# Performance work log

Measured on AMD Instinct MI355X. Metric: run time of the kernel, lower is better.

Reference implementation:

```python
import jax, jax.numpy as jnp
import numpy as np

B, T, D, HD = 256, 256, 512, 64  # batch, seq_len(SEQ_LEN), EMBED_DIM, head_dim


def setup_inputs() -> dict:
    key = jax.random.key(0)
    k1, k2, k3, k4 = jax.random.split(key, 4)
    scale = D ** -0.5  # roughly matches nn.Linear init variance
    return {
        "x": jax.random.normal(k1, (B, T, D), dtype=jnp.float32),
        "Wq": jax.random.normal(k2, (HD, D), dtype=jnp.float32) * scale,
        "Wk": jax.random.normal(k3, (HD, D), dtype=jnp.float32) * scale,
        "Wv": jax.random.normal(k4, (HD, D), dtype=jnp.float32) * scale,
    }


def reference(x, Wq, Wk, Wv):
    # q,k,v: [B, T, HD]  (torch Linear: x @ W.T, no bias)
    q = jnp.einsum("btd,hd->bth", x, Wq)
    k = jnp.einsum("btd,hd->bth", x, Wk)
    v = jnp.einsum("btd,hd->bth", x, Wv)
    head_dim = Wq.shape[0]
    # scores: [B, T, T], scaled by head_dim^-0.5
    scores = jnp.einsum("bqh,bkh->bqk", q, k) * (head_dim ** -0.5)
    T_ = x.shape[1]
    causal = jnp.tril(jnp.ones((T_, T_), dtype=bool))  # tril[:T,:T] == 0 -> -inf
    scores = jnp.where(causal, scores, -jnp.inf)
    attn = jax.nn.softmax(scores, axis=-1)
    # dropout is identity in eval mode (reference baseline)
    return jnp.einsum("bqk,bkh->bqh", attn, v)
```

## Files before the change

kernel.cpp:

```cpp
#include <hip/hip_runtime.h>
#include <hip/hip_bf16.h>
#include <stdint.h>

#define NB 256
#define NT 256
#define ND 512
#define NH 64

typedef __bf16 bf16;
typedef __bf16 bf16x4 __attribute__((ext_vector_type(4)));
typedef __bf16 bf16x8 __attribute__((ext_vector_type(8)));
typedef float f32x4 __attribute__((ext_vector_type(4)));

static __device__ __forceinline__ f32x4 mfma16(bf16x8 a, bf16x8 b, f32x4 c) {
    return __builtin_amdgcn_mfma_f32_16x16x32_bf16(a, b, c, 0, 0, 0);
}

static __device__ __forceinline__ bf16x8 cvt8(f32x4 a, f32x4 b) {
    bf16x8 r;
    r[0] = (bf16)a.x; r[1] = (bf16)a.y; r[2] = (bf16)a.z; r[3] = (bf16)a.w;
    r[4] = (bf16)b.x; r[5] = (bf16)b.y; r[6] = (bf16)b.z; r[7] = (bf16)b.w;
    return r;
}

__global__ __launch_bounds__(256) void wconv_kernel(
        const float* __restrict__ Wq, const float* __restrict__ Wk,
        const float* __restrict__ Wv, bf16* __restrict__ wbf) {
    int idx = (blockIdx.x * 256 + threadIdx.x) * 4;
    const float* src;
    if (idx < 64 * ND)       src = Wq + idx;
    else if (idx < 128 * ND) src = Wk + (idx - 64 * ND);
    else                     src = Wv + (idx - 128 * ND);
    f32x4 v = *reinterpret_cast<const f32x4*>(src);
    bf16x4 o;
    o[0] = (bf16)v.x; o[1] = (bf16)v.y; o[2] = (bf16)v.z; o[3] = (bf16)v.w;
    *reinterpret_cast<bf16x4*>(wbf + idx) = o;
}

__global__ __launch_bounds__(256) void qkv_gemm_kernel(
        const float* __restrict__ x, const bf16* __restrict__ wbf,
        bf16* __restrict__ qws, bf16* __restrict__ kws, bf16* __restrict__ vt) {
    __shared__ alignas(16) char lds[16384];
    const int t = threadIdx.x;
    const int lane = t & 63, wave = t >> 6;
    const long m0 = (long)blockIdx.x * 64;

    const int srow = t >> 2, skc = (t & 3) * 16;
    const int ssw = (srow & 7) << 4;
    const int sbase = srow * 128 + skc * 2;
    const float* xsrc = x + (m0 + srow) * ND + skc;

    f32x4 acc[4][3] = {};

    {
        f32x4 a = *reinterpret_cast<const f32x4*>(xsrc);
        f32x4 b = *reinterpret_cast<const f32x4*>(xsrc + 4);
        f32x4 c = *reinterpret_cast<const f32x4*>(xsrc + 8);
        f32x4 d = *reinterpret_cast<const f32x4*>(xsrc + 12);
        *reinterpret_cast<bf16x8*>(lds + (sbase ^ ssw)) = cvt8(a, b);
        *reinterpret_cast<bf16x8*>(lds + ((sbase + 16) ^ ssw)) = cvt8(c, d);
    }
    __syncthreads();

    #pragma unroll
    for (int kk = 0; kk < ND; kk += 64) {
        char* cbuf = lds + ((kk >> 6) & 1) * 8192;
        char* nbuf = lds + ((((kk >> 6) & 1)) ^ 1) * 8192;
        f32x4 xa, xb, xc, xd;
        const bool have_next = (kk + 64) < ND;
        if (have_next) {
            const float* s2 = xsrc + kk + 64;
            xa = *reinterpret_cast<const f32x4*>(s2);
            xb = *reinterpret_cast<const f32x4*>(s2 + 4);
            xc = *reinterpret_cast<const f32x4*>(s2 + 8);
            xd = *reinterpret_cast<const f32x4*>(s2 + 12);
        }
        #pragma unroll
        for (int k2 = 0; k2 < 2; ++k2) {
            const int koff = (k2 * 32 + (lane >> 4) * 8) * 2;
            const int kg = kk + k2 * 32 + (lane >> 4) * 8;
            bf16x8 Af[4];
            #pragma unroll
            for (int ri = 0; ri < 4; ++ri) {
                int row = ri * 16 + (lane & 15);
                Af[ri] = *reinterpret_cast<const bf16x8*>(
                    cbuf + ((row * 128 + koff) ^ ((row & 7) << 4)));
            }
            #pragma unroll
            for (int ci = 0; ci < 3; ++ci) {
                int n = wave * 48 + ci * 16 + (lane & 15);
                bf16x8 Bf = *reinterpret_cast<const bf16x8*>(wbf + n * ND + kg);
                #pragma unroll
                for (int ri = 0; ri < 4; ++ri)
                    acc[ri][ci] = mfma16(Af[ri], Bf, acc[ri][ci]);
            }
        }
        if (have_next) {
            *reinterpret_cast<bf16x8*>(nbuf + (sbase ^ ssw)) = cvt8(xa, xb);
            *reinterpret_cast<bf16x8*>(nbuf + ((sbase + 16) ^ ssw)) = cvt8(xc, xd);
        }
        __syncthreads();
    }

    const int b = blockIdx.x >> 2;
    const int tb = (blockIdx.x & 3) * 64;
    #pragma unroll
    for (int ci = 0; ci < 3; ++ci) {
        int n = wave * 48 + ci * 16 + (lane & 15);
        int sel = n >> 6, hd = n & 63;
        #pragma unroll
        for (int ri = 0; ri < 4; ++ri) {
            #pragma unroll
            for (int r = 0; r < 4; ++r) {
                int trow = tb + ri * 16 + (lane >> 4) * 4 + r;
                long grow = m0 + ri * 16 + (lane >> 4) * 4 + r;
                float val = acc[ri][ci][r];
                if (sel == 0)      qws[grow * NH + hd] = (bf16)(val * 0.125f);
                else if (sel == 1) kws[grow * NH + hd] = (bf16)val;
                else               vt[((long)b * NH + hd) * NT + trow] = (bf16)val;
            }
        }
    }
}

__global__ __launch_bounds__(256) void attn_kernel(
        const bf16* __restrict__ qws, const bf16* __restrict__ kws,
        const bf16* __restrict__ vt, float* __restrict__ out) {
    __shared__ alignas(16) char lds[32768];
    const int t = threadIdx.x, lane = t & 63, wave = t >> 6;
    const int qb = blockIdx.x, b = blockIdx.y;
    const long bbase = (long)b * NT;

    const int ncolt = qb * 4 + wave + 1;
    const int ncolt2 = (ncolt + 1) & ~1;

    bf16x8 Qf[2];
    {
        long qrow = bbase + qb * 64 + wave * 16 + (lane & 15);
        const bf16* qsrc = qws + qrow * NH + (lane >> 4) * 8;
        Qf[0] = *reinterpret_cast<const bf16x8*>(qsrc);
        Qf[1] = *reinterpret_cast<const bf16x8*>(qsrc + 32);
    }

    f32x4 S[16] = {};
    #pragma unroll
    for (int c = 0; c < 16; ++c) {
        if (c < ncolt2) {
            const bf16* kbase = kws + (bbase + c * 16 + (lane & 15)) * NH + (lane >> 4) * 8;
            S[c] = mfma16(Qf[0], *reinterpret_cast<const bf16x8*>(kbase), S[c]);
            S[c] = mfma16(Qf[1], *reinterpret_cast<const bf16x8*>(kbase + 32), S[c]);
        }
    }

    const int qrow0 = qb * 64 + wave * 16 + (lane >> 4) * 4;
    float sum[4] = {0.f, 0.f, 0.f, 0.f};
    #pragma unroll
    for (int c = 0; c < 16; ++c) {
        if (c < ncolt2) {
            int col = c * 16 + (lane & 15);
            #pragma unroll
            for (int r = 0; r < 4; ++r) {
                float p = (col <= qrow0 + r) ? __expf(S[c][r]) : 0.0f;
                S[c][r] = p;
                sum[r] += p;
            }
        }
    }
    #pragma unroll
    for (int r = 0; r < 4; ++r) {
        sum[r] += __shfl_xor(sum[r], 1);
        sum[r] += __shfl_xor(sum[r], 2);
        sum[r] += __shfl_xor(sum[r], 4);
        sum[r] += __shfl_xor(sum[r], 8);
    }

    char* plds = lds + wave * 8192;
    #pragma unroll
    for (int c = 0; c < 16; ++c) {
        if (c < ncolt2) {
            int colp = c * 16 + (lane & 15);
            #pragma unroll
            for (int r = 0; r < 4; ++r) {
                int rowp = (lane >> 4) * 4 + r;
                *reinterpret_cast<bf16*>(plds + ((rowp * 512 + colp * 2) ^ ((rowp & 7) << 4))) =
                    (bf16)S[c][r];
            }
        }
    }

    f32x4 O[4] = {};
    #pragma unroll
    for (int kk2 = 0; kk2 < 8; ++kk2) {
        if (kk2 < (ncolt2 >> 1)) {
            const int kv0 = kk2 * 32 + (lane >> 4) * 8;
            const int rowp = lane & 15;
            bf16x8 Pf = *reinterpret_cast<const bf16x8*>(
                plds + ((rowp * 512 + kv0 * 2) ^ ((rowp & 7) << 4)));
            #pragma unroll
            for (int cb = 0; cb < 4; ++cb) {
                int hd = cb * 16 + (lane & 15);
                bf16x8 Vf = *reinterpret_cast<const bf16x8*>(
                    vt + ((long)b * NH + hd) * NT + kv0);
                O[cb] = mfma16(Pf, Vf, O[cb]);
            }
        }
    }

    float rinv[4];
    #pragma unroll
    for (int r = 0; r < 4; ++r) rinv[r] = 1.0f / sum[r];

    #pragma unroll
    for (int cb = 0; cb < 4; ++cb) {
        int hd = cb * 16 + (lane & 15);
        #pragma unroll
        for (int r = 0; r < 4; ++r) {
            long orow = bbase + qb * 64 + wave * 16 + (lane >> 4) * 4 + r;
            out[orow * NH + hd] = O[cb][r] * rinv[r];
        }
    }
}

extern "C" void kernel_launch(void* const* d_in, const int* in_sizes, int n_in,
                              void* d_out, int out_size, void* d_ws, size_t ws_size,
                              hipStream_t stream) {
    const float* x  = (const float*)d_in[0];
    const float* Wq = (const float*)d_in[1];
    const float* Wk = (const float*)d_in[2];
    const float* Wv = (const float*)d_in[3];
    float* out = (float*)d_out;

    char* ws = (char*)d_ws;
    bf16* wbf = (bf16*)ws;
    bf16* qws = (bf16*)(ws + 0x30000);
    bf16* kws = (bf16*)(ws + 0x30000 + 8388608);
    bf16* vt  = (bf16*)(ws + 0x30000 + 2 * 8388608);

    wconv_kernel<<<96, 256, 0, stream>>>(Wq, Wk, Wv, wbf);
    qkv_gemm_kernel<<<1024, 256, 0, stream>>>(x, wbf, qws, kws, vt);
    attn_kernel<<<dim3(4, NB), 256, 0, stream>>>(qws, kws, vt, out);
}
```

Measured before the change: 261.9 us.

## Stage full x tile in LDS for QKV GEMM; split attention into one-wave blocks

The QKV projection now loads and converts the whole 64x512 x tile into a 64KB LDS buffer up front, then runs the MFMA loop with no per-step barriers, replacing the double-buffered loop. The attention kernel now launches one 64-thread block per 16-row query tile (16x256 grid) and fuses scoring, exp, P staging and PV accumulation into one chunked loop, avoiding the 16-register score array. This is meant to cut synchronisation and register pressure and to balance the causal workload across more blocks. The 64KB LDS allocation limits GEMM occupancy, and the staging loses overlap of the load with compute.

```diff
diff --git a/kernel.cpp b/kernel.cpp
--- a/kernel.cpp
+++ b/kernel.cpp
@@ -40,73 +40,56 @@
 __global__ __launch_bounds__(256) void qkv_gemm_kernel(
         const float* __restrict__ x, const bf16* __restrict__ wbf,
         bf16* __restrict__ qws, bf16* __restrict__ kws, bf16* __restrict__ vt) {
-    __shared__ alignas(16) char lds[16384];
+    __shared__ alignas(16) char lds[65536];
     const int t = threadIdx.x;
     const int lane = t & 63, wave = t >> 6;
     const long m0 = (long)blockIdx.x * 64;
 
-    const int srow = t >> 2, skc = (t & 3) * 16;
-    const int ssw = (srow & 7) << 4;
-    const int sbase = srow * 128 + skc * 2;
-    const float* xsrc = x + (m0 + srow) * ND + skc;
+    {
+        const int srow = t >> 2, skc = (t & 3) * 16;
+        const int ssw = (srow & 7) << 4;
+        const float* xsrc = x + (m0 + srow) * ND + skc;
+        #pragma unroll
+        for (int kk = 0; kk < ND; kk += 64) {
+            f32x4 a = *reinterpret_cast<const f32x4*>(xsrc + kk);
+            f32x4 b = *reinterpret_cast<const f32x4*>(xsrc + kk + 4);
+            f32x4 c = *reinterpret_cast<const f32x4*>(xsrc + kk + 8);
+            f32x4 d = *reinterpret_cast<const f32x4*>(xsrc + kk + 12);
+            int base = srow * 1024 + (kk + skc) * 2;
+            *reinterpret_cast<bf16x8*>(lds + (base ^ ssw)) = cvt8(a, b);
+            *reinterpret_cast<bf16x8*>(lds + ((base + 16) ^ ssw)) = cvt8(c, d);
+        }
+    }
+    __syncthreads();
 
     f32x4 acc[4][3] = {};
-
-    {
-        f32x4 a = *reinterpret_cast<const f32x4*>(xsrc);
-        f32x4 b = *reinterpret_cast<const f32x4*>(xsrc + 4);
-        f32x4 c = *reinterpret_cast<const f32x4*>(xsrc + 8);
-        f32x4 d = *reinterpret_cast<const f32x4*>(xsrc + 12);
-        *reinterpret_cast<bf16x8*>(lds + (sbase ^ ssw)) = cvt8(a, b);
-        *reinterpret_cast<bf16x8*>(lds + ((sbase + 16) ^ ssw)) = cvt8(c, d);
-    }
-    __syncthreads();
-
-    #pragma unroll
-    for (int kk = 0; kk < ND; kk += 64) {
-        char* cbuf = lds + ((kk >> 6) & 1) * 8192;
-        char* nbuf = lds + ((((kk >> 6) & 1)) ^ 1) * 8192;
-        f32x4 xa, xb, xc, xd;
-        const bool have_next = (kk + 64) < ND;
-        if (have_next) {
-            const float* s2 = xsrc + kk + 64;
-            xa = *reinterpret_cast<const f32x4*>(s2);
-            xb = *reinterpret_cast<const f32x4*>(s2 + 4);
-            xc = *reinterpret_cast<const f32x4*>(s2 + 8);
-            xd = *reinterpret_cast<const f32x4*>(s2 + 12);
-        }
-        #pragma unroll
-        for (int k2 = 0; k2 < 2; ++k2) {
-            const int koff = (k2 * 32 + (lane >> 4) * 8) * 2;
-            const int kg = kk + k2 * 32 + (lane >> 4) * 8;
-            bf16x8 Af[4];
-            #pragma unroll
-            for (int ri = 0; ri < 4; ++ri) {
-                int row = ri * 16 + (lane & 15);
-                Af[ri] = *reinterpret_cast<const bf16x8*>(
-                    cbuf + ((row * 128 + koff) ^ ((row & 7) << 4)));
-            }
-            #pragma unroll
-            for (int ci = 0; ci < 3; ++ci) {
-                int n = wave * 48 + ci * 16 + (lane & 15);
-                bf16x8 Bf = *reinterpret_cast<const bf16x8*>(wbf + n * ND + kg);
-                #pragma unroll
-                for (int ri = 0; ri < 4; ++ri)
-                    acc[ri][ci] = mfma16(Af[ri], Bf, acc[ri][ci]);
-            }
-        }
-        if (have_next) {
-            *reinterpret_cast<bf16x8*>(nbuf + (sbase ^ ssw)) = cvt8(xa, xb);
-            *reinterpret_cast<bf16x8*>(nbuf + ((sbase + 16) ^ ssw)) = cvt8(xc, xd);
-        }
-        __syncthreads();
+    const int l15 = lane & 15, g8 = (lane >> 4) * 8;
+
+    #pragma unroll 4
+    for (int chunk = 0; chunk < 16; ++chunk) {
+        const int kg = chunk * 32 + g8;
+        bf16x8 Af[4];
+        #pragma unroll
+        for (int ri = 0; ri < 4; ++ri) {
+            int row = ri * 16 + l15;
+            Af[ri] = *reinterpret_cast<const bf16x8*>(
+                lds + ((row * 1024 + kg * 2) ^ ((row & 7) << 4)));
+        }
+        #pragma unroll
+        for (int ci = 0; ci < 3; ++ci) {
+            int n = wave * 48 + ci * 16 + l15;
+            bf16x8 Bf = *reinterpret_cast<const bf16x8*>(wbf + n * ND + kg);
+            #pragma unroll
+            for (int ri = 0; ri < 4; ++ri)
+                acc[ri][ci] = mfma16(Af[ri], Bf, acc[ri][ci]);
+        }
     }
 
     const int b = blockIdx.x >> 2;
     const int tb = (blockIdx.x & 3) * 64;
     #pragma unroll
     for (int ci = 0; ci < 3; ++ci) {
-        int n = wave * 48 + ci * 16 + (lane & 15);
+        int n = wave * 48 + ci * 16 + l15;
         int sel = n >> 6, hd = n & 63;
         #pragma unroll
         for (int ri = 0; ri < 4; ++ri) {
@@ -123,100 +106,87 @@
     }
 }
 
-__global__ __launch_bounds__(256) void attn_kernel(
+__global__ __launch_bounds__(64) void attn_kernel(
         const bf16* __restrict__ qws, const bf16* __restrict__ kws,
         const bf16* __restrict__ vt, float* __restrict__ out) {
-    __shared__ alignas(16) char lds[32768];
-    const int t = threadIdx.x, lane = t & 63, wave = t >> 6;
-    const int qb = blockIdx.x, b = blockIdx.y;
+    __shared__ alignas(16) char plds[8192];
+    const int lane = threadIdx.x & 63;
+    const int l15 = lane & 15, g = lane >> 4;
+    const int qt = blockIdx.x, b = blockIdx.y;
     const long bbase = (long)b * NT;
 
-    const int ncolt = qb * 4 + wave + 1;
-    const int ncolt2 = (ncolt + 1) & ~1;
+    const int nct = qt + 1;
+    const int nch = (nct + 1) >> 1;
 
     bf16x8 Qf[2];
     {
-        long qrow = bbase + qb * 64 + wave * 16 + (lane & 15);
-        const bf16* qsrc = qws + qrow * NH + (lane >> 4) * 8;
+        long qrow = bbase + qt * 16 + l15;
+        const bf16* qsrc = qws + qrow * NH + g * 8;
         Qf[0] = *reinterpret_cast<const bf16x8*>(qsrc);
         Qf[1] = *reinterpret_cast<const bf16x8*>(qsrc + 32);
     }
 
-    f32x4 S[16] = {};
-    #pragma unroll
-    for (int c = 0; c < 16; ++c) {
-        if (c < ncolt2) {
-            const bf16* kbase = kws + (bbase + c * 16 + (lane & 15)) * NH + (lane >> 4) * 8;
-            S[c] = mfma16(Qf[0], *reinterpret_cast<const bf16x8*>(kbase), S[c]);
-            S[c] = mfma16(Qf[1], *reinterpret_cast<const bf16x8*>(kbase + 32), S[c]);
-        }
-    }
-
-    const int qrow0 = qb * 64 + wave * 16 + (lane >> 4) * 4;
+    const int qrow0 = qt * 16 + g * 4;
     float sum[4] = {0.f, 0.f, 0.f, 0.f};
-    #pragma unroll
-    for (int c = 0; c < 16; ++c) {
-        if (c < ncolt2) {
-            int col = c * 16 + (lane & 15);
+    f32x4 O[4] = {};
+
+    #pragma unroll
+    for (int ch = 0; ch < 8; ++ch) {
+        if (ch < nch) {
+            const int t0 = 2 * ch, t1 = 2 * ch + 1;
+            const bool t1v = (t1 < nct);
+            f32x4 S0 = {}, S1 = {};
+            {
+                const bf16* kb0 = kws + (bbase + t0 * 16 + l15) * NH + g * 8;
+                S0 = mfma16(Qf[0], *reinterpret_cast<const bf16x8*>(kb0), S0);
+                S0 = mfma16(Qf[1], *reinterpret_cast<const bf16x8*>(kb0 + 32), S0);
+                if (t1v) {
+                    const bf16* kb1 = kb0 + 16 * NH;
+                    S1 = mfma16(Qf[0], *reinterpret_cast<const bf16x8*>(kb1), S1);
+                    S1 = mfma16(Qf[1], *reinterpret_cast<const bf16x8*>(kb1 + 32), S1);
+                }
+            }
+            const int c0 = t0 * 16 + l15, c1 = c0 + 16;
             #pragma unroll
             for (int r = 0; r < 4; ++r) {
-                float p = (col <= qrow0 + r) ? __expf(S[c][r]) : 0.0f;
-                S[c][r] = p;
-                sum[r] += p;
-            }
-        }
-    }
+                int rowp = g * 4 + r;
+                int sw = (rowp & 7) << 4;
+                float p0 = (c0 <= qrow0 + r) ? __expf(S0[r]) : 0.0f;
+                sum[r] += p0;
+                *reinterpret_cast<bf16*>(plds + ((rowp * 512 + c0 * 2) ^ sw)) = (bf16)p0;
+                float p1 = (t1v && c1 <= qrow0 + r) ? __expf(S1[r]) : 0.0f;
+                sum[r] += p1;
+                *reinterpret_cast<bf16*>(plds + ((rowp * 512 + c1 * 2) ^ sw)) = (bf16)p1;
+            }
+            const int k0 = ch * 32 + g * 8;
+            bf16x8 Pf = *reinterpret_cast<const bf16x8*>(
+                plds + ((l15 * 512 + k0 * 2) ^ ((l15 & 7) << 4)));
+            #pragma unroll
+            for (int cb = 0; cb < 4; ++cb) {
+                int hd = cb * 16 + l15;
+                bf16x8 Vf = *reinterpret_cast<const bf16x8*>(
+                    vt + ((long)b * NH + hd) * NT + k0);
+                O[cb] = mfma16(Pf, Vf, O[cb]);
+            }
+        }
+    }
+
     #pragma unroll
     for (int r = 0; r < 4; ++r) {
         sum[r] += __shfl_xor(sum[r], 1);
         sum[r] += __shfl_xor(sum[r], 2);
         sum[r] += __shfl_xor(sum[r], 4);
         sum[r] += __shfl_xor(sum[r], 8);
-    }
-
-    char* plds = lds + wave * 8192;
-    #pragma unroll
-    for (int c = 0; c < 16; ++c) {
-        if (c < ncolt2) {
-            int colp = c * 16 + (lane & 15);
-            #pragma unroll
-            for (int r = 0; r < 4; ++r) {
-                int rowp = (lane >> 4) * 4 + r;
-                *reinterpret_cast<bf16*>(plds + ((rowp * 512 + colp * 2) ^ ((rowp & 7) << 4))) =
-                    (bf16)S[c][r];
-            }
-        }
-    }
-
-    f32x4 O[4] = {};
-    #pragma unroll
-    for (int kk2 = 0; kk2 < 8; ++kk2) {
-        if (kk2 < (ncolt2 >> 1)) {
-            const int kv0 = kk2 * 32 + (lane >> 4) * 8;
-            const int rowp = lane & 15;
-            bf16x8 Pf = *reinterpret_cast<const bf16x8*>(
-                plds + ((rowp * 512 + kv0 * 2) ^ ((rowp & 7) << 4)));
-            #pragma unroll
-            for (int cb = 0; cb < 4; ++cb) {
-                int hd = cb * 16 + (lane & 15);
-                bf16x8 Vf = *reinterpret_cast<const bf16x8*>(
-                    vt + ((long)b * NH + hd) * NT + kv0);
-                O[cb] = mfma16(Pf, Vf, O[cb]);
-            }
-        }
-    }
-
-    float rinv[4];
-    #pragma unroll
-    for (int r = 0; r < 4; ++r) rinv[r] = 1.0f / sum[r];
+        sum[r] = 1.0f / sum[r];
+    }
 
     #pragma unroll
     for (int cb = 0; cb < 4; ++cb) {
-        int hd = cb * 16 + (lane & 15);
+        int hd = cb * 16 + l15;
         #pragma unroll
         for (int r = 0; r < 4; ++r) {
-            long orow = bbase + qb * 64 + wave * 16 + (lane >> 4) * 4 + r;
-            out[orow * NH + hd] = O[cb][r] * rinv[r];
+            long orow = bbase + qt * 16 + g * 4 + r;
+            out[orow * NH + hd] = O[cb][r] * sum[r];
         }
     }
 }
@@ -238,5 +208,5 @@
 
     wconv_kernel<<<96, 256, 0, stream>>>(Wq, Wk, Wv, wbf);
     qkv_gemm_kernel<<<1024, 256, 0, stream>>>(x, wbf, qws, kws, vt);
-    attn_kernel<<<dim3(4, NB), 256, 0, stream>>>(qws, kws, vt, out);
-}
+    attn_kernel<<<dim3(16, NB), 64, 0, stream>>>(qws, kws, vt, out);
+}
```

Result: no change. 259.1 us (-1.1%).
